# Optimization experiments

Hardware: AMD Instinct MI355X
Metric: run time of the kernel (lower is better)

## Reference

```python
import jax, jax.numpy as jnp
import numpy as np
from jax import lax

STATE_LEN = 5
N_BASE = 4
N_STATES = N_BASE ** STATE_LEN      # 1024
ALPHA_LEN = N_BASE + 1              # 5 (blank + 4 bases)
BLANK_SCORE = 2.0
SCALE = 5.0
NEG = -1e30                         # log-zero surrogate (avoids -inf NaNs)

def _make_idx():
    s = np.arange(N_STATES)
    stay = s[:, None]
    # torch: arange(1024).repeat_interleave(4).reshape(4,-1).T -> idx[j,1+b] = b*256 + j//4
    move = np.repeat(s, N_BASE).reshape(N_BASE, -1).T
    return jnp.asarray(np.concatenate([stay, move], axis=1), dtype=jnp.int32)  # (1024,5)

IDX = _make_idx()

def _logZ_full(scores):
    # full-lattice logZ; scores (T,N,5120)
    T, N, C = scores.shape
    Ms = scores.reshape(T, N, N_STATES, ALPHA_LEN)
    def step(alpha, Mt):
        a = alpha[:, IDX]                          # (N,1024,5) gather of predecessors
        return jax.nn.logsumexp(a + Mt, axis=-1), None
    alpha0 = jnp.zeros((N, N_STATES), scores.dtype)
    alphaT, _ = lax.scan(step, alpha0, Ms)
    return jax.nn.logsumexp(alphaT, axis=-1)       # (N,)

def _prepare_ctc_scores(scores, targets):
    # scores (T,N,C), targets (N,Lmax) base ids in 1..4
    t = jnp.clip(targets - 1, 0)
    T, N, C = scores.shape
    Lmax = t.shape[1]
    n = Lmax - (STATE_LEN - 1)
    stay_idx = sum(t[:, i:n + i] * (N_BASE ** (STATE_LEN - i - 1)) for i in range(STATE_LEN)) * ALPHA_LEN
    move_idx = stay_idx[:, 1:] + t[:, :n - 1] + 1
    stay = jnp.take_along_axis(scores, jnp.broadcast_to(stay_idx[None], (T, N, n)), axis=2)
    move = jnp.take_along_axis(scores, jnp.broadcast_to(move_idx[None], (T, N, n - 1)), axis=2)
    return stay, move

def _ctc_logZ(stay, move, lens):
    # stay (T,N,L), move (T,N,L-1), lens (N,) effective kmer-path lengths
    T, N, L = stay.shape
    alpha0 = jnp.full((N, L), NEG, stay.dtype).at[:, 0].set(0.0)
    def step(alpha, sm):
        s, m = sm
        moved = jnp.pad(alpha[:, :-1] + m, ((0, 0), (1, 0)), constant_values=NEG)
        return jnp.logaddexp(alpha + s, moved), None
    alphaT, _ = lax.scan(step, alpha0, (stay, move))
    return alphaT[jnp.arange(N), lens - 1]

def setup_inputs() -> dict:
    key = jax.random.key(0)
    k1, k2, k3, k4, k5, k6 = jax.random.split(key, 6)
    B, T, D, Lmax = 16, 512, 512, 256
    hs_pad = jax.random.normal(k1, (B, T, D), dtype=jnp.float32)
    hlens = jnp.full((B,), T, dtype=jnp.int32)
    ys_pad = jax.random.randint(k2, (B, Lmax), 1, 5, dtype=jnp.int32)
    ys_lens = jax.random.randint(k3, (B,), 64, Lmax + 1, dtype=jnp.int32)
    W = jax.random.normal(k4, (4096, D), dtype=jnp.float32) * 0.02
    b = jax.random.normal(k5, (4096,), dtype=jnp.float32) * 0.01
    return {"hs_pad": hs_pad, "hlens": hlens, "ys_pad": ys_pad, "ys_lens": ys_lens, "W": W, "b": b}

def reference(hs_pad, hlens, ys_pad, ys_lens, W, b):
    x = jnp.transpose(hs_pad, (1, 0, 2))                 # (T,B,D)
    scores = jnp.tanh(x @ W.T + b) * SCALE               # (T,N,4096)
    T, N, C = scores.shape
    scores = jnp.pad(scores.reshape(T, N, C // N_BASE, N_BASE),
                     ((0, 0), (0, 0), (0, 0), (1, 0)), constant_values=BLANK_SCORE)
    scores = scores.reshape(T, N, -1).astype(jnp.float32)  # (T,N,5120)
    # normalise: subtract full-lattice logZ / T
    logZ = _logZ_full(scores)
    norm = scores - logZ[:, None] / T                    # (N,1) broadcasts over (T,N,C)
    stay, move = _prepare_ctc_scores(norm, ys_pad)
    logz = _ctc_logZ(stay, move, ys_lens + 1 - STATE_LEN)
    loss = -(logz / ys_lens.astype(scores.dtype))        # (N,) (reduction=None in forward)
    scores_bt = jnp.transpose(scores, (1, 0, 2))
    return loss, scores_bt, scores_bt
```

## Files before the change

kernel.cpp:

```cpp
#include <hip/hip_runtime.h>
#include <hip/hip_bf16.h>
#include <hip/hip_fp16.h>
#include <math.h>

#define T_STEPS 512
#define NB      16
#define D_IN    512
#define CG      4096
#define CO      5120
#define NSTATES 1024
#define LMAX    252
#define NEGF    (-1e30f)
#define SCORES_SZ 41943040LL
#define L2E 1.4426950408889634f
#define LN2 0.6931471805599453f

typedef __attribute__((ext_vector_type(8))) short bf16x8;
typedef __attribute__((ext_vector_type(4))) float f32x4;

__device__ __forceinline__ float tanh5(float x) {
    x = fminf(fmaxf(x, -15.f), 15.f);
    float e = __expf(2.f * x);
    return 5.f * (e - 1.f) / (e + 1.f);
}
__device__ __forceinline__ unsigned short f2bf(float v) {
    __hip_bfloat16 h = __float2bfloat16(v);
    return *reinterpret_cast<unsigned short*>(&h);
}
__device__ __forceinline__ float h2f(unsigned short s) {
    union { unsigned short u; _Float16 h; } c; c.u = s;
    return (float)c.h;
}
__device__ __forceinline__ unsigned short f2h(float v) {
    union { unsigned short u; _Float16 h; } c; c.h = (_Float16)v;
    return c.u;
}

__global__ __launch_bounds__(256) void cvt_bf16_kernel(const float* __restrict__ src,
                                                       unsigned short* __restrict__ dst,
                                                       int n4) {
    int i = blockIdx.x * 256 + threadIdx.x;
    if (i < n4) {
        float4 v = *(reinterpret_cast<const float4*>(src) + i);
        ushort4 o;
        o.x = f2bf(v.x); o.y = f2bf(v.y); o.z = f2bf(v.z); o.w = f2bf(v.w);
        *(reinterpret_cast<ushort4*>(dst) + i) = o;
    }
}

template <bool WSE>
__global__ __launch_bounds__(256) void crf_gemm_bf16(
    const unsigned short* __restrict__ A16,
    const unsigned short* __restrict__ W16,
    const float* __restrict__ bias,
    float* __restrict__ out,
    unsigned short* __restrict__ e16)
{
    __shared__ unsigned short As[128 * 64];
    __shared__ unsigned short Bs[128 * 64];
    const int tid  = threadIdx.x;
    const int lane = tid & 63;
    const int wv   = __builtin_amdgcn_readfirstlane(tid >> 6);
    const int wr   = wv >> 1, wc = wv & 1;
    const int m0   = blockIdx.y * 128;
    const int n0   = blockIdx.x * 128;
    const int wbase = tid & 192;

    f32x4 acc[4][4];
    #pragma unroll
    for (int i = 0; i < 4; ++i)
        #pragma unroll
        for (int j = 0; j < 4; ++j) acc[i][j] = (f32x4){0.f, 0.f, 0.f, 0.f};

    const int l15 = lane & 15, lj = lane >> 4, l7 = lane & 7;

    for (int k0 = 0; k0 < D_IN; k0 += 64) {
        __syncthreads();
        #pragma unroll
        for (int i = 0; i < 4; ++i) {
            const int c   = i * 256 + tid;
            const int row = c >> 3;
            const int jg  = (c & 7) ^ (row & 7);
            const unsigned short* ga = A16 + (size_t)(m0 + row) * D_IN + k0 + jg * 8;
            const unsigned short* gb = W16 + (size_t)(n0 + row) * D_IN + k0 + jg * 8;
            unsigned short* la = As + (size_t)(i * 256 + wbase) * 8;
            unsigned short* lb = Bs + (size_t)(i * 256 + wbase) * 8;
            __builtin_amdgcn_global_load_lds((const __attribute__((address_space(1))) void*)ga,
                                             (__attribute__((address_space(3))) void*)la, 16, 0, 0);
            __builtin_amdgcn_global_load_lds((const __attribute__((address_space(1))) void*)gb,
                                             (__attribute__((address_space(3))) void*)lb, 16, 0, 0);
        }
        __syncthreads();
        #pragma unroll
        for (int ks = 0; ks < 2; ++ks) {
            bf16x8 af[4], bb[4];
            #pragma unroll
            for (int mi = 0; mi < 4; ++mi) {
                const int row = wr * 64 + mi * 16 + l15;
                const int jsw = (ks * 4 + lj) ^ l7;
                af[mi] = *reinterpret_cast<const bf16x8*>(&As[row * 64 + jsw * 8]);
            }
            #pragma unroll
            for (int ni = 0; ni < 4; ++ni) {
                const int row = wc * 64 + ni * 16 + l15;
                const int jsw = (ks * 4 + lj) ^ l7;
                bb[ni] = *reinterpret_cast<const bf16x8*>(&Bs[row * 64 + jsw * 8]);
            }
            #pragma unroll
            for (int mi = 0; mi < 4; ++mi)
                #pragma unroll
                for (int ni = 0; ni < 4; ++ni)
                    acc[mi][ni] = __builtin_amdgcn_mfma_f32_16x16x32_bf16(
                        af[mi], bb[ni], acc[mi][ni], 0, 0, 0);
        }
    }

    float bv[4];
    #pragma unroll
    for (int ni = 0; ni < 4; ++ni) bv[ni] = bias[n0 + wc * 64 + ni * 16 + l15];

    #pragma unroll
    for (int mi = 0; mi < 4; ++mi) {
        #pragma unroll
        for (int r = 0; r < 4; ++r) {
            const int m = m0 + wr * 64 + mi * 16 + lj * 4 + r;
            float* r1 = out + 16 + (size_t)m * CO;
            #pragma unroll
            for (int ni = 0; ni < 4; ++ni) {
                const int n = n0 + wc * 64 + ni * 16 + l15;
                const float v = tanh5(acc[mi][ni][r] + bv[ni]);
                const int ch = (n >> 2) * 5 + (n & 3) + 1;
                r1[ch] = v;
                r1[ch + SCORES_SZ] = v;
                if ((l15 & 3) == 0) {
                    r1[ch - 1] = 2.0f;
                    r1[ch - 1 + SCORES_SZ] = 2.0f;
                }
                if (WSE) e16[(size_t)m * CG + n] = f2h(__expf(v));
            }
        }
    }
}

__device__ __forceinline__ void cvt8(uint4 u, float* g) {
    g[0] = h2f((unsigned short)(u.x & 0xffff)); g[1] = h2f((unsigned short)(u.x >> 16));
    g[2] = h2f((unsigned short)(u.y & 0xffff)); g[3] = h2f((unsigned short)(u.y >> 16));
    g[4] = h2f((unsigned short)(u.z & 0xffff)); g[5] = h2f((unsigned short)(u.z >> 16));
    g[6] = h2f((unsigned short)(u.w & 0xffff)); g[7] = h2f((unsigned short)(u.w >> 16));
}

__global__ __launch_bounds__(256) void fwd_pd_kernel(
    const unsigned short* __restrict__ e16,
    const int* __restrict__ ys_pad,
    const int* __restrict__ ys_lens,
    float* __restrict__ ws)
{
    const int blk = blockIdx.x;
    if (blk < NB) {
        const int n = blk;
        const int q = threadIdx.x;
        const int lane = q & 63, wvi = q >> 6;
        __shared__ float buf[2][NSTATES];
        __shared__ float red[256];
        __shared__ float wmax4[4];
        const float e2 = 7.38905609893065f;
        float P0 = 1.f, P1 = 1.f, P2 = 1.f, P3 = 1.f;
        float acc = 0.f;
        *(float4*)&buf[0][4 * q] = make_float4(1.f, 1.f, 1.f, 1.f);
        const unsigned short* base = e16 + (size_t)(n * T_STEPS) * CG + 16 * q;
        uint4 pf[4][2];
        #pragma unroll
        for (int u = 0; u < 4; ++u) {
            pf[u][0] = *reinterpret_cast<const uint4*>(base + (size_t)u * CG);
            pf[u][1] = *reinterpret_cast<const uint4*>(base + (size_t)u * CG + 8);
        }
        __syncthreads();
        int cur = 0;
        for (int t = 0; t < T_STEPS; t += 8) {
            #pragma unroll
            for (int u = 0; u < 8; ++u) {
                float g[16];
                cvt8(pf[u & 3][0], g);
                cvt8(pf[u & 3][1], g + 8);
                int tp = t + u + 4; if (tp > T_STEPS - 1) tp = T_STEPS - 1;
                const unsigned short* rp = base + (size_t)tp * CG;
                pf[u & 3][0] = *reinterpret_cast<const uint4*>(rp);
                pf[u & 3][1] = *reinterpret_cast<const uint4*>(rp + 8);
                const float b0 = buf[cur][q];
                const float b1 = buf[cur][q + 256];
                const float b2 = buf[cur][q + 512];
                const float b3 = buf[cur][q + 768];
                float n0 = fmaf(e2, P0, fmaf(g[0],  b0, g[1]  * b1) + fmaf(g[2],  b2, g[3]  * b3));
                float n1 = fmaf(e2, P1, fmaf(g[4],  b0, g[5]  * b1) + fmaf(g[6],  b2, g[7]  * b3));
                float n2 = fmaf(e2, P2, fmaf(g[8],  b0, g[9]  * b1) + fmaf(g[10], b2, g[11] * b3));
                float n3 = fmaf(e2, P3, fmaf(g[12], b0, g[13] * b1) + fmaf(g[14], b2, g[15] * b3));
                if (u == 1) {
                    const float wm = fmaxf(fmaxf(wmax4[0], wmax4[1]), fmaxf(wmax4[2], wmax4[3]));
                    const int e = (int)((__float_as_uint(wm) >> 23) & 0xff) - 127;
                    const float c = __uint_as_float((unsigned)(127 - e) << 23);
                    n0 *= c; n1 *= c; n2 *= c; n3 *= c;
                    acc += (float)e;
                }
                P0 = n0; P1 = n1; P2 = n2; P3 = n3;
                *(float4*)&buf[cur ^ 1][4 * q] = make_float4(P0, P1, P2, P3);
                if (u == 0) {
                    float lm = fmaxf(fmaxf(P0, P1), fmaxf(P2, P3));
                    #pragma unroll
                    for (int msk = 1; msk < 64; msk <<= 1)
                        lm = fmaxf(lm, __shfl_xor(lm, msk, 64));
                    if (lane == 0) wmax4[wvi] = lm;
                }
                __syncthreads();
                cur ^= 1;
            }
        }
        red[q] = (P0 + P1) + (P2 + P3);
        __syncthreads();
        for (int off = 128; off > 0; off >>= 1) {
            if (q < off) red[q] += red[q + off];
            __syncthreads();
        }
        if (q == 0) ws[n] = LN2 * (acc + __builtin_amdgcn_logf(red[0]));
    } else {
        const int n = blk - NB;
        const int i = threadIdx.x;
        const float STAY = 2.0f * L2E;
        __shared__ float abuf[2][LMAX];
        __shared__ int tcl[256];
        if (i < 256) tcl[i] = max(ys_pad[n * 256 + i] - 1, 0);
        __syncthreads();
        int mch = -1;
        if (i >= 1 && i < LMAX) {
            const int code = tcl[i] * 256 + tcl[i + 1] * 64 + tcl[i + 2] * 16
                           + tcl[i + 3] * 4 + tcl[i + 4];
            mch = code * 4 + tcl[i - 1];
        }
        float alpha = (i == 0) ? 0.f : NEGF;
        if (i < LMAX) abuf[0][i] = alpha;
        const unsigned short* base = e16 + (size_t)(n * T_STEPS) * CG;
        const size_t moff = (mch >= 0) ? (size_t)mch : 0;
        float pg[4];
        #pragma unroll
        for (int u = 0; u < 4; ++u) pg[u] = h2f(base[(size_t)u * CG + moff]);
        __syncthreads();
        int cur = 0;
        for (int t = 0; t < T_STEPS; t += 4) {
            #pragma unroll
            for (int u = 0; u < 4; ++u) {
                const float g2 = __builtin_amdgcn_logf(pg[u]);
                int tp = t + u + 4; if (tp > T_STEPS - 1) tp = T_STEPS - 1;
                pg[u] = h2f(base[(size_t)tp * CG + moff]);
                if (i < LMAX) {
                    const float a_stay = alpha + STAY;
                    const float prev = (i > 0) ? abuf[cur][i - 1] : NEGF;
                    const float a_mv = (i > 0) ? (prev + g2) : NEGF;
                    const float mx = fmaxf(a_stay, a_mv);
                    const float mn = fminf(a_stay, a_mv);
                    alpha = mx + __builtin_amdgcn_logf(1.f + __builtin_amdgcn_exp2f(mn - mx));
                    abuf[cur ^ 1][i] = alpha;
                }
                __syncthreads();
                cur ^= 1;
            }
        }
        if (i == ys_lens[n] - 5) ws[NB + n] = alpha * LN2;
    }
}

__global__ __launch_bounds__(1024) void crf_fwd_kernel(
    const float* __restrict__ scores,
    const int* __restrict__ ys_pad,
    const int* __restrict__ ys_lens,
    float* __restrict__ ws)
{
    const int blk = blockIdx.x;
    const float STAY = 2.0f * L2E;
    if (blk < NB) {
        const int n = blk;
        const int s = threadIdx.x;
        __shared__ float buf[2][NSTATES];
        __shared__ float red[NSTATES];
        float alpha = 0.f;
        buf[0][s] = 0.f;
        const int j0 = s >> 2;
        const float* rowp = scores + (size_t)(n * T_STEPS) * CO + 5 * s + 1;
        float pm[4][4];
        #pragma unroll
        for (int u = 0; u < 4; ++u) {
            const float* r = rowp + (size_t)u * CO;
            pm[u][0] = r[0]; pm[u][1] = r[1]; pm[u][2] = r[2]; pm[u][3] = r[3];
        }
        __syncthreads();
        int cur = 0;
        for (int t = 0; t < T_STEPS; t += 4) {
            #pragma unroll
            for (int u = 0; u < 4; ++u) {
                const float m1 = pm[u][0], m2 = pm[u][1], m3 = pm[u][2], m4 = pm[u][3];
                int tp = t + u + 4; if (tp > T_STEPS - 1) tp = T_STEPS - 1;
                const float* r = rowp + (size_t)tp * CO;
                pm[u][0] = r[0]; pm[u][1] = r[1]; pm[u][2] = r[2]; pm[u][3] = r[3];
                const float b1 = buf[cur][j0];
                const float b2 = buf[cur][j0 + 256];
                const float b3 = buf[cur][j0 + 512];
                const float b4 = buf[cur][j0 + 768];
                const float a0 = alpha + STAY;
                const float a1 = fmaf(m1, L2E, b1);
                const float a2 = fmaf(m2, L2E, b2);
                const float a3 = fmaf(m3, L2E, b3);
                const float a4 = fmaf(m4, L2E, b4);
                const float mx = fmaxf(fmaxf(fmaxf(a0, a1), fmaxf(a2, a3)), a4);
                const float sum = __builtin_amdgcn_exp2f(a0 - mx) + __builtin_amdgcn_exp2f(a1 - mx)
                                + __builtin_amdgcn_exp2f(a2 - mx) + __builtin_amdgcn_exp2f(a3 - mx)
                                + __builtin_amdgcn_exp2f(a4 - mx);
                alpha = mx + __builtin_amdgcn_logf(sum);
                buf[cur ^ 1][s] = alpha;
                __syncthreads();
                cur ^= 1;
            }
        }
        red[s] = alpha;
        __syncthreads();
        for (int off = 512; off > 0; off >>= 1) {
            if (s < off) red[s] = fmaxf(red[s], red[s + off]);
            __syncthreads();
        }
        const float gmax = red[0];
        __syncthreads();
        red[s] = __builtin_amdgcn_exp2f(alpha - gmax);
        __syncthreads();
        for (int off = 512; off > 0; off >>= 1) {
            if (s < off) red[s] += red[s + off];
            __syncthreads();
        }
        if (s == 0) ws[n] = LN2 * (gmax + __builtin_amdgcn_logf(red[0]));
    } else {
        const int n = blk - NB;
        const int i = threadIdx.x;
        __shared__ float abuf[2][LMAX];
        __shared__ int tcl[256];
        if (i < 256) tcl[i] = max(ys_pad[n * 256 + i] - 1, 0);
        __syncthreads();
        int mch = -1;
        if (i >= 1 && i < LMAX) {
            const int code = tcl[i] * 256 + tcl[i + 1] * 64 + tcl[i + 2] * 16
                           + tcl[i + 3] * 4 + tcl[i + 4];
            mch = code * 5 + tcl[i - 1] + 1;
        }
        float alpha = (i == 0) ? 0.f : NEGF;
        if (i < LMAX) abuf[0][i] = alpha;
        const float* base = scores + (size_t)(n * T_STEPS) * CO;
        const size_t moff = (mch >= 0) ? (size_t)mch : 0;
        float pg[4];
        #pragma unroll
        for (int u = 0; u < 4; ++u) pg[u] = base[(size_t)u * CO + moff];
        __syncthreads();
        int cur = 0;
        for (int t = 0; t < T_STEPS; t += 4) {
            #pragma unroll
            for (int u = 0; u < 4; ++u) {
                const float g = pg[u];
                int tp = t + u + 4; if (tp > T_STEPS - 1) tp = T_STEPS - 1;
                pg[u] = base[(size_t)tp * CO + moff];
                if (i < LMAX) {
                    const float a_stay = alpha + STAY;
                    const float prev = (i > 0) ? abuf[cur][i - 1] : NEGF;
                    const float a_mv = (i > 0) ? fmaf(g, L2E, prev) : NEGF;
                    const float mx = fmaxf(a_stay, a_mv);
                    const float mn = fminf(a_stay, a_mv);
                    alpha = mx + __builtin_amdgcn_logf(1.f + __builtin_amdgcn_exp2f(mn - mx));
                    abuf[cur ^ 1][i] = alpha;
                }
                __syncthreads();
                cur ^= 1;
            }
        }
        if (i == ys_lens[n] - 5) ws[NB + n] = alpha * LN2;
    }
}

__global__ void crf_loss_kernel(const float* __restrict__ ws,
                                const int* __restrict__ ys_lens,
                                float* __restrict__ out)
{
    const int n = threadIdx.x;
    if (n < NB) {
        const float logz = ws[NB + n] - ws[n];
        out[n] = -(logz / (float)ys_lens[n]);
    }
}

extern "C" void kernel_launch(void* const* d_in, const int* in_sizes, int n_in,
                              void* d_out, int out_size, void* d_ws, size_t ws_size,
                              hipStream_t stream)
{
    const float* hs      = (const float*)d_in[0];
    const int*   ys_pad  = (const int*)d_in[2];
    const int*   ys_lens = (const int*)d_in[3];
    const float* W       = (const float*)d_in[4];
    const float* bias    = (const float*)d_in[5];
    float* out = (float*)d_out;
    float* ws  = (float*)d_ws;

    const size_t A_ELEMS = (size_t)8192 * 512;
    const size_t W_ELEMS = (size_t)4096 * 512;
    const size_t S_ELEMS = (size_t)8192 * 4096;
    const size_t NEED2 = 256 + (A_ELEMS + W_ELEMS) * 2 + S_ELEMS * 2;

    unsigned short* A16 = (unsigned short*)((char*)d_ws + 256);
    unsigned short* W16 = A16 + A_ELEMS;
    unsigned short* E16 = W16 + W_ELEMS;

    cvt_bf16_kernel<<<(int)(A_ELEMS / 4 / 256), 256, 0, stream>>>(hs, A16, (int)(A_ELEMS / 4));
    cvt_bf16_kernel<<<(int)(W_ELEMS / 4 / 256), 256, 0, stream>>>(W, W16, (int)(W_ELEMS / 4));
    dim3 grid(CG / 128, (NB * T_STEPS) / 128);

    if (ws_size >= NEED2) {
        crf_gemm_bf16<true><<<grid, 256, 0, stream>>>(A16, W16, bias, out, E16);
        fwd_pd_kernel<<<2 * NB, 256, 0, stream>>>(E16, ys_pad, ys_lens, ws);
    } else {
        crf_gemm_bf16<false><<<grid, 256, 0, stream>>>(A16, W16, bias, out, nullptr);
        crf_fwd_kernel<<<2 * NB, 1024, 0, stream>>>(out + 16, ys_pad, ys_lens, ws);
    }
    crf_loss_kernel<<<1, 64, 0, stream>>>(ws, ys_lens, out);
}
```

Measured before the change: 240.2 us.

## Run CRF forward recursions in a single wavefront with packed fp16 dot products

Replaces the 256-thread forward kernel with a one-wavefront-per-sequence kernel. Each lane holds 16 states, the previous alpha is kept as packed fp16 in LDS, and the update uses fdot2. This removes the per-step block barriers and the cross-wave max reduction. The exp scores are pre-shifted by -3 so they fit in fp16, and renormalisation uses a lagged exponent. The CTC path now has each lane handle four positions with a shuffle for the neighbour and deeper prefetch. In exchange it adds fp16 precision risk to the alpha state and gives fewer threads for latency hiding.

```diff
diff --git a/kernel.cpp b/kernel.cpp
--- a/kernel.cpp
+++ b/kernel.cpp
@@ -8,7 +8,6 @@
 #define D_IN    512
 #define CG      4096
 #define CO      5120
-#define NSTATES 1024
 #define LMAX    252
 #define NEGF    (-1e30f)
 #define SCORES_SZ 41943040LL
@@ -17,6 +16,7 @@
 
 typedef __attribute__((ext_vector_type(8))) short bf16x8;
 typedef __attribute__((ext_vector_type(4))) float f32x4;
+typedef _Float16 h16x2 __attribute__((ext_vector_type(2)));
 
 __device__ __forceinline__ float tanh5(float x) {
     x = fminf(fmaxf(x, -15.f), 15.f);
@@ -34,6 +34,20 @@
 __device__ __forceinline__ unsigned short f2h(float v) {
     union { unsigned short u; _Float16 h; } c; c.h = (_Float16)v;
     return c.u;
+}
+__device__ __forceinline__ float fdot2u(unsigned int a, unsigned int b, float c) {
+#if __has_builtin(__builtin_amdgcn_fdot2)
+    return __builtin_amdgcn_fdot2(__builtin_bit_cast(h16x2, a),
+                                  __builtin_bit_cast(h16x2, b), c, false);
+#else
+    float r = c;
+    r = fmaf(h2f((unsigned short)(a & 0xffff)), h2f((unsigned short)(b & 0xffff)), r);
+    r = fmaf(h2f((unsigned short)(a >> 16)),    h2f((unsigned short)(b >> 16)),    r);
+    return r;
+#endif
+}
+__device__ __forceinline__ unsigned int pk16(float a, float b) {
+    return __builtin_bit_cast(unsigned int, __builtin_amdgcn_cvt_pkrtz(a, b));
 }
 
 __global__ __launch_bounds__(256) void cvt_bf16_kernel(const float* __restrict__ src,
@@ -136,134 +150,174 @@
                     r1[ch - 1] = 2.0f;
                     r1[ch - 1 + SCORES_SZ] = 2.0f;
                 }
-                if (WSE) e16[(size_t)m * CG + n] = f2h(__expf(v));
-            }
-        }
-    }
-}
-
-__device__ __forceinline__ void cvt8(uint4 u, float* g) {
-    g[0] = h2f((unsigned short)(u.x & 0xffff)); g[1] = h2f((unsigned short)(u.x >> 16));
-    g[2] = h2f((unsigned short)(u.y & 0xffff)); g[3] = h2f((unsigned short)(u.y >> 16));
-    g[4] = h2f((unsigned short)(u.z & 0xffff)); g[5] = h2f((unsigned short)(u.z >> 16));
-    g[6] = h2f((unsigned short)(u.w & 0xffff)); g[7] = h2f((unsigned short)(u.w >> 16));
-}
-
-__global__ __launch_bounds__(256) void fwd_pd_kernel(
+                if (WSE) e16[(size_t)m * CG + n] = f2h(__expf(v - 3.0f));
+            }
+        }
+    }
+}
+
+__global__ __launch_bounds__(64) void fwd_wave_kernel(
     const unsigned short* __restrict__ e16,
     const int* __restrict__ ys_pad,
     const int* __restrict__ ys_lens,
     float* __restrict__ ws)
 {
     const int blk = blockIdx.x;
+    const int L = threadIdx.x;
+    const float STAYT = 0.36787944117144233f;
     if (blk < NB) {
         const int n = blk;
-        const int q = threadIdx.x;
-        const int lane = q & 63, wvi = q >> 6;
-        __shared__ float buf[2][NSTATES];
-        __shared__ float red[256];
-        __shared__ float wmax4[4];
-        const float e2 = 7.38905609893065f;
-        float P0 = 1.f, P1 = 1.f, P2 = 1.f, P3 = 1.f;
+        __shared__ unsigned int Bsh[512];
+        float P[4][4];
+        #pragma unroll
+        for (int d = 0; d < 4; ++d)
+            #pragma unroll
+            for (int k = 0; k < 4; ++k) P[d][k] = 1.f;
+        {
+            const unsigned int one2 = 0x3C003C00u;
+            uint4 w; w.x = one2; w.y = one2; w.z = one2; w.w = one2;
+            *reinterpret_cast<uint4*>(&Bsh[4 * L]) = w;
+            *reinterpret_cast<uint4*>(&Bsh[256 + 4 * L]) = w;
+        }
         float acc = 0.f;
-        *(float4*)&buf[0][4 * q] = make_float4(1.f, 1.f, 1.f, 1.f);
-        const unsigned short* base = e16 + (size_t)(n * T_STEPS) * CG + 16 * q;
-        uint4 pf[4][2];
-        #pragma unroll
-        for (int u = 0; u < 4; ++u) {
-            pf[u][0] = *reinterpret_cast<const uint4*>(base + (size_t)u * CG);
-            pf[u][1] = *reinterpret_cast<const uint4*>(base + (size_t)u * CG + 8);
-        }
-        __syncthreads();
-        int cur = 0;
-        for (int t = 0; t < T_STEPS; t += 8) {
-            #pragma unroll
-            for (int u = 0; u < 8; ++u) {
-                float g[16];
-                cvt8(pf[u & 3][0], g);
-                cvt8(pf[u & 3][1], g + 8);
+        int ei_m1 = 0, ei_m2 = 0;
+        const unsigned short* gb = e16 + (size_t)(n * T_STEPS) * CG + 16 * L;
+        uint4 gq[4][4][2];
+        #pragma unroll
+        for (int u = 0; u < 4; ++u)
+            #pragma unroll
+            for (int k = 0; k < 4; ++k) {
+                gq[u][k][0] = *reinterpret_cast<const uint4*>(gb + (size_t)u * CG + 1024 * k);
+                gq[u][k][1] = *reinterpret_cast<const uint4*>(gb + (size_t)u * CG + 1024 * k + 8);
+            }
+        for (int t = 0; t < T_STEPS; t += 4) {
+            #pragma unroll
+            for (int u = 0; u < 4; ++u) {
+                unsigned int b01[4], b23[4];
+                #pragma unroll
+                for (int k = 0; k < 4; ++k) {
+                    b01[k] = Bsh[L + 64 * k];
+                    b23[k] = Bsh[256 + L + 64 * k];
+                }
+                const float c = __uint_as_float((unsigned)(127 - ei_m2) << 23);
+                acc += (float)ei_m2;
+                float nv[4][4];
+                #pragma unroll
+                for (int k = 0; k < 4; ++k) {
+                    const uint4 q0 = gq[u][k][0];
+                    const uint4 q1 = gq[u][k][1];
+                    nv[0][k] = fdot2u(q0.x, b01[k], fdot2u(q0.y, b23[k], STAYT * P[0][k])) * c;
+                    nv[1][k] = fdot2u(q0.z, b01[k], fdot2u(q0.w, b23[k], STAYT * P[1][k])) * c;
+                    nv[2][k] = fdot2u(q1.x, b01[k], fdot2u(q1.y, b23[k], STAYT * P[2][k])) * c;
+                    nv[3][k] = fdot2u(q1.z, b01[k], fdot2u(q1.w, b23[k], STAYT * P[3][k])) * c;
+                }
                 int tp = t + u + 4; if (tp > T_STEPS - 1) tp = T_STEPS - 1;
-                const unsigned short* rp = base + (size_t)tp * CG;
-                pf[u & 3][0] = *reinterpret_cast<const uint4*>(rp);
-                pf[u & 3][1] = *reinterpret_cast<const uint4*>(rp + 8);
-                const float b0 = buf[cur][q];
-                const float b1 = buf[cur][q + 256];
-                const float b2 = buf[cur][q + 512];
-                const float b3 = buf[cur][q + 768];
-                float n0 = fmaf(e2, P0, fmaf(g[0],  b0, g[1]  * b1) + fmaf(g[2],  b2, g[3]  * b3));
-                float n1 = fmaf(e2, P1, fmaf(g[4],  b0, g[5]  * b1) + fmaf(g[6],  b2, g[7]  * b3));
-                float n2 = fmaf(e2, P2, fmaf(g[8],  b0, g[9]  * b1) + fmaf(g[10], b2, g[11] * b3));
-                float n3 = fmaf(e2, P3, fmaf(g[12], b0, g[13] * b1) + fmaf(g[14], b2, g[15] * b3));
-                if (u == 1) {
-                    const float wm = fmaxf(fmaxf(wmax4[0], wmax4[1]), fmaxf(wmax4[2], wmax4[3]));
-                    const int e = (int)((__float_as_uint(wm) >> 23) & 0xff) - 127;
-                    const float c = __uint_as_float((unsigned)(127 - e) << 23);
-                    n0 *= c; n1 *= c; n2 *= c; n3 *= c;
-                    acc += (float)e;
-                }
-                P0 = n0; P1 = n1; P2 = n2; P3 = n3;
-                *(float4*)&buf[cur ^ 1][4 * q] = make_float4(P0, P1, P2, P3);
-                if (u == 0) {
-                    float lm = fmaxf(fmaxf(P0, P1), fmaxf(P2, P3));
+                #pragma unroll
+                for (int k = 0; k < 4; ++k) {
+                    gq[u][k][0] = *reinterpret_cast<const uint4*>(gb + (size_t)tp * CG + 1024 * k);
+                    gq[u][k][1] = *reinterpret_cast<const uint4*>(gb + (size_t)tp * CG + 1024 * k + 8);
+                }
+                #pragma unroll
+                for (int d = 0; d < 4; ++d)
                     #pragma unroll
-                    for (int msk = 1; msk < 64; msk <<= 1)
-                        lm = fmaxf(lm, __shfl_xor(lm, msk, 64));
-                    if (lane == 0) wmax4[wvi] = lm;
-                }
-                __syncthreads();
-                cur ^= 1;
-            }
-        }
-        red[q] = (P0 + P1) + (P2 + P3);
-        __syncthreads();
-        for (int off = 128; off > 0; off >>= 1) {
-            if (q < off) red[q] += red[q + off];
-            __syncthreads();
-        }
-        if (q == 0) ws[n] = LN2 * (acc + __builtin_amdgcn_logf(red[0]));
+                    for (int k = 0; k < 4; ++k) P[d][k] = nv[d][k];
+                uint4 w01, w23;
+                w01.x = pk16(P[0][0], P[0][1]); w01.y = pk16(P[1][0], P[1][1]);
+                w01.z = pk16(P[2][0], P[2][1]); w01.w = pk16(P[3][0], P[3][1]);
+                w23.x = pk16(P[0][2], P[0][3]); w23.y = pk16(P[1][2], P[1][3]);
+                w23.z = pk16(P[2][2], P[2][3]); w23.w = pk16(P[3][2], P[3][3]);
+                *reinterpret_cast<uint4*>(&Bsh[4 * L]) = w01;
+                *reinterpret_cast<uint4*>(&Bsh[256 + 4 * L]) = w23;
+                float m = P[0][0];
+                #pragma unroll
+                for (int d = 0; d < 4; ++d)
+                    #pragma unroll
+                    for (int k = 0; k < 4; ++k) m = fmaxf(m, P[d][k]);
+                #pragma unroll
+                for (int msk = 1; msk < 64; msk <<= 1)
+                    m = fmaxf(m, __shfl_xor(m, msk, 64));
+                int e; (void)frexpf(m, &e);
+                ei_m2 = ei_m1; ei_m1 = e;
+            }
+        }
+        float s = 0.f;
+        #pragma unroll
+        for (int d = 0; d < 4; ++d)
+            #pragma unroll
+            for (int k = 0; k < 4; ++k) s += P[d][k];
+        #pragma unroll
+        for (int msk = 1; msk < 64; msk <<= 1)
+            s += __shfl_xor(s, msk, 64);
+        if (L == 0) ws[n] = LN2 * (acc + __builtin_amdgcn_logf(s));
     } else {
         const int n = blk - NB;
-        const int i = threadIdx.x;
-        const float STAY = 2.0f * L2E;
-        __shared__ float abuf[2][LMAX];
         __shared__ int tcl[256];
-        if (i < 256) tcl[i] = max(ys_pad[n * 256 + i] - 1, 0);
-        __syncthreads();
-        int mch = -1;
-        if (i >= 1 && i < LMAX) {
-            const int code = tcl[i] * 256 + tcl[i + 1] * 64 + tcl[i + 2] * 16
-                           + tcl[i + 3] * 4 + tcl[i + 4];
-            mch = code * 4 + tcl[i - 1];
-        }
-        float alpha = (i == 0) ? 0.f : NEGF;
-        if (i < LMAX) abuf[0][i] = alpha;
-        const unsigned short* base = e16 + (size_t)(n * T_STEPS) * CG;
-        const size_t moff = (mch >= 0) ? (size_t)mch : 0;
-        float pg[4];
-        #pragma unroll
-        for (int u = 0; u < 4; ++u) pg[u] = h2f(base[(size_t)u * CG + moff]);
-        __syncthreads();
-        int cur = 0;
-        for (int t = 0; t < T_STEPS; t += 4) {
-            #pragma unroll
-            for (int u = 0; u < 4; ++u) {
-                const float g2 = __builtin_amdgcn_logf(pg[u]);
-                int tp = t + u + 4; if (tp > T_STEPS - 1) tp = T_STEPS - 1;
-                pg[u] = h2f(base[(size_t)tp * CG + moff]);
-                if (i < LMAX) {
-                    const float a_stay = alpha + STAY;
-                    const float prev = (i > 0) ? abuf[cur][i - 1] : NEGF;
-                    const float a_mv = (i > 0) ? (prev + g2) : NEGF;
-                    const float mx = fmaxf(a_stay, a_mv);
-                    const float mn = fminf(a_stay, a_mv);
-                    alpha = mx + __builtin_amdgcn_logf(1.f + __builtin_amdgcn_exp2f(mn - mx));
-                    abuf[cur ^ 1][i] = alpha;
-                }
-                __syncthreads();
-                cur ^= 1;
-            }
-        }
-        if (i == ys_lens[n] - 5) ws[NB + n] = alpha * LN2;
+        #pragma unroll
+        for (int r = 0; r < 4; ++r)
+            tcl[4 * L + r] = max(ys_pad[n * 256 + 4 * L + r] - 1, 0);
+        __syncthreads();
+        int mch[4]; bool val[4];
+        #pragma unroll
+        for (int d = 0; d < 4; ++d) {
+            const int i = 4 * L + d;
+            val[d] = (i >= 1 && i < LMAX);
+            if (val[d]) {
+                const int code = tcl[i] * 256 + tcl[i + 1] * 64 + tcl[i + 2] * 16
+                               + tcl[i + 3] * 4 + tcl[i + 4];
+                mch[d] = code * 4 + tcl[i - 1];
+            } else mch[d] = 0;
+        }
+        const unsigned short* eb = e16 + (size_t)(n * T_STEPS) * CG;
+        unsigned short pv[8][4];
+        #pragma unroll
+        for (int u = 0; u < 8; ++u)
+            #pragma unroll
+            for (int d = 0; d < 4; ++d)
+                pv[u][d] = eb[(size_t)u * CG + mch[d]];
+        float a[4];
+        a[0] = (L == 0) ? 0.f : NEGF;
+        a[1] = NEGF; a[2] = NEGF; a[3] = NEGF;
+        const float STAY2 = (2.0f - 3.0f) * L2E;
+        for (int t = 0; t < T_STEPS; t += 8) {
+            #pragma unroll
+            for (int u = 0; u < 8; ++u) {
+                float g2[4];
+                #pragma unroll
+                for (int d = 0; d < 4; ++d)
+                    g2[d] = val[d] ? __builtin_amdgcn_logf(h2f(pv[u][d])) : NEGF;
+                int tp = t + u + 8; if (tp > T_STEPS - 1) tp = T_STEPS - 1;
+                #pragma unroll
+                for (int d = 0; d < 4; ++d)
+                    pv[u][d] = eb[(size_t)tp * CG + mch[d]];
+                float pA = __shfl_up(a[3], 1, 64);
+                if (L == 0) pA = NEGF;
+                const float prev0 = pA, prev1 = a[0], prev2 = a[1], prev3 = a[2];
+                {
+                    const float st = a[0] + STAY2, mv = prev0 + g2[0];
+                    const float mx = fmaxf(st, mv), mn = fminf(st, mv);
+                    a[0] = mx + __builtin_amdgcn_logf(1.f + __builtin_amdgcn_exp2f(mn - mx));
+                }
+                {
+                    const float st = a[1] + STAY2, mv = prev1 + g2[1];
+                    const float mx = fmaxf(st, mv), mn = fminf(st, mv);
+                    a[1] = mx + __builtin_amdgcn_logf(1.f + __builtin_amdgcn_exp2f(mn - mx));
+                }
+                {
+                    const float st = a[2] + STAY2, mv = prev2 + g2[2];
+                    const float mx = fmaxf(st, mv), mn = fminf(st, mv);
+                    a[2] = mx + __builtin_amdgcn_logf(1.f + __builtin_amdgcn_exp2f(mn - mx));
+                }
+                {
+                    const float st = a[3] + STAY2, mv = prev3 + g2[3];
+                    const float mx = fmaxf(st, mv), mn = fminf(st, mv);
+                    a[3] = mx + __builtin_amdgcn_logf(1.f + __builtin_amdgcn_exp2f(mn - mx));
+                }
+            }
+        }
+        const int li = ys_lens[n] - 5;
+        #pragma unroll
+        for (int d = 0; d < 4; ++d)
+            if (4 * L + d == li) ws[NB + n] = LN2 * a[d];
     }
 }
 
@@ -278,8 +332,8 @@
     if (blk < NB) {
         const int n = blk;
         const int s = threadIdx.x;
-        __shared__ float buf[2][NSTATES];
-        __shared__ float red[NSTATES];
+        __shared__ float buf[2][1024];
+        __shared__ float red[1024];
         float alpha = 0.f;
         buf[0][s] = 0.f;
         const int j0 = s >> 2;
@@ -403,8 +457,8 @@
 
     const size_t A_ELEMS = (size_t)8192 * 512;
     const size_t W_ELEMS = (size_t)4096 * 512;
-    const size_t S_ELEMS = (size_t)8192 * 4096;
-    const size_t NEED2 = 256 + (A_ELEMS + W_ELEMS) * 2 + S_ELEMS * 2;
+    const size_t E_ELEMS = (size_t)8192 * 4096;
+    const size_t NEED = 256 + (A_ELEMS + W_ELEMS + E_ELEMS) * 2;
 
     unsigned short* A16 = (unsigned short*)((char*)d_ws + 256);
     unsigned short* W16 = A16 + A_ELEMS;
@@ -414,9 +468,9 @@
     cvt_bf16_kernel<<<(int)(W_ELEMS / 4 / 256), 256, 0, stream>>>(W, W16, (int)(W_ELEMS / 4));
     dim3 grid(CG / 128, (NB * T_STEPS) / 128);
 
-    if (ws_size >= NEED2) {
+    if (ws_size >= NEED) {
         crf_gemm_bf16<true><<<grid, 256, 0, stream>>>(A16, W16, bias, out, E16);
-        fwd_pd_kernel<<<2 * NB, 256, 0, stream>>>(E16, ys_pad, ys_lens, ws);
+        fwd_wave_kernel<<<2 * NB, 64, 0, stream>>>(E16, ys_pad, ys_lens, ws);
     } else {
         crf_gemm_bf16<false><<<grid, 256, 0, stream>>>(A16, W16, bias, out, nullptr);
         crf_fwd_kernel<<<2 * NB, 1024, 0, stream>>>(out + 16, ys_pad, ys_lens, ws);
```

Result: slower. 356.4 us (+48.4%).

## Split sequential CRF and CTC recurrences into forward and backward halves

Applied to the files above, without the earlier changes.

The full-lattice and CTC alpha recurrences now run as a forward pass over the first 256 steps and a backward (beta) pass over the last 256 steps in separate blocks. A new combine kernel joins them with a dot product for the full lattice and a logsumexp for the CTC lattice. This halves the serial dependency chain that bounds the sequential scan. It also shifts the exp scores by -3 to keep fp16 in range and replaces __syncthreads with a lighter lgkmcnt-wait barrier. The cost is an extra kernel launch and some global traffic for the intermediate vectors, and the backward CTC uses a different boundary setup that must match the reference semantics.

```diff
diff --git a/kernel.cpp b/kernel.cpp
--- a/kernel.cpp
+++ b/kernel.cpp
@@ -8,12 +8,12 @@
 #define D_IN    512
 #define CG      4096
 #define CO      5120
-#define NSTATES 1024
 #define LMAX    252
 #define NEGF    (-1e30f)
 #define SCORES_SZ 41943040LL
 #define L2E 1.4426950408889634f
 #define LN2 0.6931471805599453f
+#define STAYT 0.36787944117144233f
 
 typedef __attribute__((ext_vector_type(8))) short bf16x8;
 typedef __attribute__((ext_vector_type(4))) float f32x4;
@@ -34,6 +34,17 @@
 __device__ __forceinline__ unsigned short f2h(float v) {
     union { unsigned short u; _Float16 h; } c; c.h = (_Float16)v;
     return c.u;
+}
+__device__ __forceinline__ void cvt8(uint4 u, float* g) {
+    g[0] = h2f((unsigned short)(u.x & 0xffff)); g[1] = h2f((unsigned short)(u.x >> 16));
+    g[2] = h2f((unsigned short)(u.y & 0xffff)); g[3] = h2f((unsigned short)(u.y >> 16));
+    g[4] = h2f((unsigned short)(u.z & 0xffff)); g[5] = h2f((unsigned short)(u.z >> 16));
+    g[6] = h2f((unsigned short)(u.w & 0xffff)); g[7] = h2f((unsigned short)(u.w >> 16));
+}
+__device__ __forceinline__ void step_barrier() {
+    asm volatile("s_waitcnt lgkmcnt(0)" ::: "memory");
+    __builtin_amdgcn_s_barrier();
+    asm volatile("" ::: "memory");
 }
 
 __global__ __launch_bounds__(256) void cvt_bf16_kernel(const float* __restrict__ src,
@@ -136,64 +147,67 @@
                     r1[ch - 1] = 2.0f;
                     r1[ch - 1 + SCORES_SZ] = 2.0f;
                 }
-                if (WSE) e16[(size_t)m * CG + n] = f2h(__expf(v));
-            }
-        }
-    }
-}
-
-__device__ __forceinline__ void cvt8(uint4 u, float* g) {
-    g[0] = h2f((unsigned short)(u.x & 0xffff)); g[1] = h2f((unsigned short)(u.x >> 16));
-    g[2] = h2f((unsigned short)(u.y & 0xffff)); g[3] = h2f((unsigned short)(u.y >> 16));
-    g[4] = h2f((unsigned short)(u.z & 0xffff)); g[5] = h2f((unsigned short)(u.z >> 16));
-    g[6] = h2f((unsigned short)(u.w & 0xffff)); g[7] = h2f((unsigned short)(u.w >> 16));
-}
-
-__global__ __launch_bounds__(256) void fwd_pd_kernel(
+                if (WSE) e16[(size_t)m * CG + n] = f2h(__expf(v - 3.0f));
+            }
+        }
+    }
+}
+
+__global__ __launch_bounds__(256) void fb_kernel(
     const unsigned short* __restrict__ e16,
     const int* __restrict__ ys_pad,
     const int* __restrict__ ys_lens,
-    float* __restrict__ ws)
+    float* __restrict__ FA, float* __restrict__ FAe,
+    float* __restrict__ FB, float* __restrict__ FBe,
+    float* __restrict__ CAL, float* __restrict__ CBE)
 {
-    const int blk = blockIdx.x;
-    if (blk < NB) {
-        const int n = blk;
-        const int q = threadIdx.x;
+    const int role = blockIdx.x >> 4;
+    const int n = blockIdx.x & 15;
+    const int q = threadIdx.x;
+    if (role < 2) {
+        __shared__ float buf[2][1024];
+        __shared__ float wmax4[4];
         const int lane = q & 63, wvi = q >> 6;
-        __shared__ float buf[2][NSTATES];
-        __shared__ float red[256];
-        __shared__ float wmax4[4];
-        const float e2 = 7.38905609893065f;
-        float P0 = 1.f, P1 = 1.f, P2 = 1.f, P3 = 1.f;
-        float acc = 0.f;
+        float P0 = 1.f, P1 = 1.f, P2 = 1.f, P3 = 1.f, acc = 0.f;
         *(float4*)&buf[0][4 * q] = make_float4(1.f, 1.f, 1.f, 1.f);
-        const unsigned short* base = e16 + (size_t)(n * T_STEPS) * CG + 16 * q;
+        const unsigned short* eb = e16 + (size_t)(n * T_STEPS) * CG + 16 * q;
+        const bool FWD = (role == 0);
         uint4 pf[4][2];
         #pragma unroll
         for (int u = 0; u < 4; ++u) {
-            pf[u][0] = *reinterpret_cast<const uint4*>(base + (size_t)u * CG);
-            pf[u][1] = *reinterpret_cast<const uint4*>(base + (size_t)u * CG + 8);
-        }
-        __syncthreads();
+            const int row = FWD ? u : (511 - u);
+            pf[u][0] = *(const uint4*)(eb + (size_t)row * CG);
+            pf[u][1] = *(const uint4*)(eb + (size_t)row * CG + 8);
+        }
+        step_barrier();
         int cur = 0;
-        for (int t = 0; t < T_STEPS; t += 8) {
+        for (int t = 0; t < 256; t += 8) {
             #pragma unroll
             for (int u = 0; u < 8; ++u) {
                 float g[16];
                 cvt8(pf[u & 3][0], g);
                 cvt8(pf[u & 3][1], g + 8);
-                int tp = t + u + 4; if (tp > T_STEPS - 1) tp = T_STEPS - 1;
-                const unsigned short* rp = base + (size_t)tp * CG;
-                pf[u & 3][0] = *reinterpret_cast<const uint4*>(rp);
-                pf[u & 3][1] = *reinterpret_cast<const uint4*>(rp + 8);
-                const float b0 = buf[cur][q];
-                const float b1 = buf[cur][q + 256];
-                const float b2 = buf[cur][q + 512];
-                const float b3 = buf[cur][q + 768];
-                float n0 = fmaf(e2, P0, fmaf(g[0],  b0, g[1]  * b1) + fmaf(g[2],  b2, g[3]  * b3));
-                float n1 = fmaf(e2, P1, fmaf(g[4],  b0, g[5]  * b1) + fmaf(g[6],  b2, g[7]  * b3));
-                float n2 = fmaf(e2, P2, fmaf(g[8],  b0, g[9]  * b1) + fmaf(g[10], b2, g[11] * b3));
-                float n3 = fmaf(e2, P3, fmaf(g[12], b0, g[13] * b1) + fmaf(g[14], b2, g[15] * b3));
+                int tn = t + u + 4; if (tn > 255) tn = 255;
+                const int row = FWD ? tn : (511 - tn);
+                pf[u & 3][0] = *(const uint4*)(eb + (size_t)row * CG);
+                pf[u & 3][1] = *(const uint4*)(eb + (size_t)row * CG + 8);
+                float n0, n1, n2, n3;
+                if (FWD) {
+                    const float b0 = buf[cur][q];
+                    const float b1 = buf[cur][q + 256];
+                    const float b2 = buf[cur][q + 512];
+                    const float b3 = buf[cur][q + 768];
+                    n0 = fmaf(STAYT, P0, fmaf(g[0],  b0, g[1]  * b1) + fmaf(g[2],  b2, g[3]  * b3));
+                    n1 = fmaf(STAYT, P1, fmaf(g[4],  b0, g[5]  * b1) + fmaf(g[6],  b2, g[7]  * b3));
+                    n2 = fmaf(STAYT, P2, fmaf(g[8],  b0, g[9]  * b1) + fmaf(g[10], b2, g[11] * b3));
+                    n3 = fmaf(STAYT, P3, fmaf(g[12], b0, g[13] * b1) + fmaf(g[14], b2, g[15] * b3));
+                } else {
+                    const float4 b4 = *(const float4*)&buf[cur][4 * q];
+                    n0 = fmaf(STAYT, P0, fmaf(g[0], b4.x, g[4] * b4.y) + fmaf(g[8],  b4.z, g[12] * b4.w));
+                    n1 = fmaf(STAYT, P1, fmaf(g[1], b4.x, g[5] * b4.y) + fmaf(g[9],  b4.z, g[13] * b4.w));
+                    n2 = fmaf(STAYT, P2, fmaf(g[2], b4.x, g[6] * b4.y) + fmaf(g[10], b4.z, g[14] * b4.w));
+                    n3 = fmaf(STAYT, P3, fmaf(g[3], b4.x, g[7] * b4.y) + fmaf(g[11], b4.z, g[15] * b4.w));
+                }
                 if (u == 1) {
                     const float wm = fmaxf(fmaxf(wmax4[0], wmax4[1]), fmaxf(wmax4[2], wmax4[3]));
                     const int e = (int)((__float_as_uint(wm) >> 23) & 0xff) - 127;
@@ -202,68 +216,132 @@
                     acc += (float)e;
                 }
                 P0 = n0; P1 = n1; P2 = n2; P3 = n3;
-                *(float4*)&buf[cur ^ 1][4 * q] = make_float4(P0, P1, P2, P3);
+                if (FWD) {
+                    *(float4*)&buf[cur ^ 1][4 * q] = make_float4(P0, P1, P2, P3);
+                } else {
+                    buf[cur ^ 1][q]       = P0;
+                    buf[cur ^ 1][q + 256] = P1;
+                    buf[cur ^ 1][q + 512] = P2;
+                    buf[cur ^ 1][q + 768] = P3;
+                }
                 if (u == 0) {
-                    float lm = fmaxf(fmaxf(P0, P1), fmaxf(P2, P3));
+                    float m = fmaxf(fmaxf(P0, P1), fmaxf(P2, P3));
                     #pragma unroll
                     for (int msk = 1; msk < 64; msk <<= 1)
-                        lm = fmaxf(lm, __shfl_xor(lm, msk, 64));
-                    if (lane == 0) wmax4[wvi] = lm;
+                        m = fmaxf(m, __shfl_xor(m, msk, 64));
+                    if (lane == 0) wmax4[wvi] = m;
                 }
-                __syncthreads();
+                step_barrier();
                 cur ^= 1;
             }
         }
-        red[q] = (P0 + P1) + (P2 + P3);
-        __syncthreads();
+        if (FWD) {
+            *(float4*)&FA[n * 1024 + 4 * q] = make_float4(P0, P1, P2, P3);
+            if (q == 0) FAe[n] = acc;
+        } else {
+            FB[n * 1024 + q]       = P0;
+            FB[n * 1024 + q + 256] = P1;
+            FB[n * 1024 + q + 512] = P2;
+            FB[n * 1024 + q + 768] = P3;
+            if (q == 0) FBe[n] = acc;
+        }
+    } else {
+        const bool FWD = (role == 2);
+        __shared__ float abuf[2][256];
+        __shared__ int tcl[256];
+        tcl[q] = max(ys_pad[n * 256 + q] - 1, 0);
+        __syncthreads();
+        int mch = 0; bool val;
+        if (FWD) {
+            val = (q >= 1 && q < LMAX);
+            if (val) {
+                const int code = tcl[q] * 256 + tcl[q + 1] * 64 + tcl[q + 2] * 16
+                               + tcl[q + 3] * 4 + tcl[q + 4];
+                mch = code * 4 + tcl[q - 1];
+            }
+        } else {
+            val = (q < LMAX - 1);
+            if (val) {
+                const int code = tcl[q + 1] * 256 + tcl[q + 2] * 64 + tcl[q + 3] * 16
+                               + tcl[q + 4] * 4 + tcl[q + 5];
+                mch = code * 4 + tcl[q];
+            }
+        }
+        const int li = ys_lens[n] - 5;
+        float a;
+        if (FWD) a = (q == 0) ? 0.f : NEGF;
+        else     a = (q == li) ? 0.f : NEGF;
+        abuf[0][q] = a;
+        const unsigned short* eb = e16 + (size_t)(n * T_STEPS) * CG;
+        unsigned short pv[8];
+        #pragma unroll
+        for (int u = 0; u < 8; ++u) {
+            const int row = FWD ? u : (511 - u);
+            pv[u] = eb[(size_t)row * CG + mch];
+        }
+        step_barrier();
+        const float STAY2 = (2.0f - 3.0f) * L2E;
+        int cur = 0;
+        for (int t = 0; t < 256; t += 8) {
+            #pragma unroll
+            for (int u = 0; u < 8; ++u) {
+                const float g2 = val ? __builtin_amdgcn_logf(h2f(pv[u])) : NEGF;
+                int tn = t + u + 8; if (tn > 255) tn = 255;
+                const int row = FWD ? tn : (511 - tn);
+                pv[u] = eb[(size_t)row * CG + mch];
+                float nb;
+                if (FWD) nb = (q > 0) ? abuf[cur][q - 1] : NEGF;
+                else     nb = (q < 255) ? abuf[cur][q + 1] : NEGF;
+                const float st = a + STAY2;
+                const float mv = nb + g2;
+                const float mx = fmaxf(st, mv);
+                const float mn = fminf(st, mv);
+                a = mx + __builtin_amdgcn_logf(1.f + __builtin_amdgcn_exp2f(mn - mx));
+                abuf[cur ^ 1][q] = a;
+                step_barrier();
+                cur ^= 1;
+            }
+        }
+        if (FWD) CAL[n * 256 + q] = a;
+        else     CBE[n * 256 + q] = a;
+    }
+}
+
+__global__ __launch_bounds__(256) void combine_kernel(
+    const float* __restrict__ FA, const float* __restrict__ FAe,
+    const float* __restrict__ FB, const float* __restrict__ FBe,
+    const float* __restrict__ CAL, const float* __restrict__ CBE,
+    float* __restrict__ ws)
+{
+    __shared__ float red[256];
+    const int q = threadIdx.x;
+    if (blockIdx.x < 16) {
+        const int n = blockIdx.x;
+        float s = 0.f;
+        #pragma unroll
+        for (int k = 0; k < 4; ++k)
+            s += FA[n * 1024 + 4 * q + k] * FB[n * 1024 + 4 * q + k];
+        red[q] = s; __syncthreads();
         for (int off = 128; off > 0; off >>= 1) {
             if (q < off) red[q] += red[q + off];
             __syncthreads();
         }
-        if (q == 0) ws[n] = LN2 * (acc + __builtin_amdgcn_logf(red[0]));
+        if (q == 0) ws[n] = LN2 * (FAe[n] + FBe[n] + __builtin_amdgcn_logf(red[0]));
     } else {
-        const int n = blk - NB;
-        const int i = threadIdx.x;
-        const float STAY = 2.0f * L2E;
-        __shared__ float abuf[2][LMAX];
-        __shared__ int tcl[256];
-        if (i < 256) tcl[i] = max(ys_pad[n * 256 + i] - 1, 0);
-        __syncthreads();
-        int mch = -1;
-        if (i >= 1 && i < LMAX) {
-            const int code = tcl[i] * 256 + tcl[i + 1] * 64 + tcl[i + 2] * 16
-                           + tcl[i + 3] * 4 + tcl[i + 4];
-            mch = code * 4 + tcl[i - 1];
-        }
-        float alpha = (i == 0) ? 0.f : NEGF;
-        if (i < LMAX) abuf[0][i] = alpha;
-        const unsigned short* base = e16 + (size_t)(n * T_STEPS) * CG;
-        const size_t moff = (mch >= 0) ? (size_t)mch : 0;
-        float pg[4];
-        #pragma unroll
-        for (int u = 0; u < 4; ++u) pg[u] = h2f(base[(size_t)u * CG + moff]);
-        __syncthreads();
-        int cur = 0;
-        for (int t = 0; t < T_STEPS; t += 4) {
-            #pragma unroll
-            for (int u = 0; u < 4; ++u) {
-                const float g2 = __builtin_amdgcn_logf(pg[u]);
-                int tp = t + u + 4; if (tp > T_STEPS - 1) tp = T_STEPS - 1;
-                pg[u] = h2f(base[(size_t)tp * CG + moff]);
-                if (i < LMAX) {
-                    const float a_stay = alpha + STAY;
-                    const float prev = (i > 0) ? abuf[cur][i - 1] : NEGF;
-                    const float a_mv = (i > 0) ? (prev + g2) : NEGF;
-                    const float mx = fmaxf(a_stay, a_mv);
-                    const float mn = fminf(a_stay, a_mv);
-                    alpha = mx + __builtin_amdgcn_logf(1.f + __builtin_amdgcn_exp2f(mn - mx));
-                    abuf[cur ^ 1][i] = alpha;
-                }
-                __syncthreads();
-                cur ^= 1;
-            }
-        }
-        if (i == ys_lens[n] - 5) ws[NB + n] = alpha * LN2;
+        const int n = blockIdx.x - 16;
+        const float x = CAL[n * 256 + q] + CBE[n * 256 + q];
+        red[q] = x; __syncthreads();
+        for (int off = 128; off > 0; off >>= 1) {
+            if (q < off) red[q] = fmaxf(red[q], red[q + off]);
+            __syncthreads();
+        }
+        const float m = red[0]; __syncthreads();
+        red[q] = __builtin_amdgcn_exp2f(x - m); __syncthreads();
+        for (int off = 128; off > 0; off >>= 1) {
+            if (q < off) red[q] += red[q + off];
+            __syncthreads();
+        }
+        if (q == 0) ws[NB + n] = LN2 * (m + __builtin_amdgcn_logf(red[0]));
     }
 }
 
@@ -278,8 +356,8 @@
     if (blk < NB) {
         const int n = blk;
         const int s = threadIdx.x;
-        __shared__ float buf[2][NSTATES];
-        __shared__ float red[NSTATES];
+        __shared__ float buf[2][1024];
+        __shared__ float red[1024];
         float alpha = 0.f;
         buf[0][s] = 0.f;
         const int j0 = s >> 2;
@@ -403,20 +481,28 @@
 
     const size_t A_ELEMS = (size_t)8192 * 512;
     const size_t W_ELEMS = (size_t)4096 * 512;
-    const size_t S_ELEMS = (size_t)8192 * 4096;
-    const size_t NEED2 = 256 + (A_ELEMS + W_ELEMS) * 2 + S_ELEMS * 2;
+    const size_t E_ELEMS = (size_t)8192 * 4096;
+    const size_t X_FLOATS = (size_t)16 * 1024 * 2 + 32 + (size_t)16 * 256 * 2;
+    const size_t NEED = 256 + (A_ELEMS + W_ELEMS + E_ELEMS) * 2 + X_FLOATS * 4;
 
     unsigned short* A16 = (unsigned short*)((char*)d_ws + 256);
     unsigned short* W16 = A16 + A_ELEMS;
     unsigned short* E16 = W16 + W_ELEMS;
+    float* FA  = (float*)(E16 + E_ELEMS);
+    float* FAe = FA + 16 * 1024;
+    float* FB  = FAe + 16;
+    float* FBe = FB + 16 * 1024;
+    float* CAL = FBe + 16;
+    float* CBE = CAL + 16 * 256;
 
     cvt_bf16_kernel<<<(int)(A_ELEMS / 4 / 256), 256, 0, stream>>>(hs, A16, (int)(A_ELEMS / 4));
     cvt_bf16_kernel<<<(int)(W_ELEMS / 4 / 256), 256, 0, stream>>>(W, W16, (int)(W_ELEMS / 4));
     dim3 grid(CG / 128, (NB * T_STEPS) / 128);
 
-    if (ws_size >= NEED2) {
+    if (ws_size >= NEED) {
         crf_gemm_bf16<true><<<grid, 256, 0, stream>>>(A16, W16, bias, out, E16);
-        fwd_pd_kernel<<<2 * NB, 256, 0, stream>>>(E16, ys_pad, ys_lens, ws);
+        fb_kernel<<<64, 256, 0, stream>>>(E16, ys_pad, ys_lens, FA, FAe, FB, FBe, CAL, CBE);
+        combine_kernel<<<32, 256, 0, stream>>>(FA, FAe, FB, FBe, CAL, CBE, ws);
     } else {
         crf_gemm_bf16<false><<<grid, 256, 0, stream>>>(A16, W16, bias, out, nullptr);
         crf_fwd_kernel<<<2 * NB, 1024, 0, stream>>>(out + 16, ys_pad, ys_lens, ws);
```

After: 220.7 us. 1.09x faster.
